# Kernel tuning notes

Hardware: AMD Instinct MI355X
Metric: run time of the kernel (lower is better)

The kernel has to match this reference:

```python
import jax, jax.numpy as jnp
import numpy as np

B, K, R = 16, 256, 256          # batch, text length, encoder dim (r_out_size)
CONV_OUT = 8                    # l_conv_out_size
SW_C = 16                       # l_swish_c_out_size
SW_W = 16                       # l_swish_w_out_size
KS = 3                          # l_conv_kernel_size
T_MAX = 1000                    # torch.clamp(pred_mel_len, max=1000) -> static frame dim
BN_EPS = 1e-5
LN_EPS = 1e-5


def _layer_norm(x, g, b):
    mu = jnp.mean(x, -1, keepdims=True)
    var = jnp.var(x, -1, keepdims=True)
    return (x - mu) * jax.lax.rsqrt(var + LN_EPS) * g + b


def _conv_block(V, w, b, bn_g, bn_b, ln_g, ln_b):
    # ConvBlock: Conv1d(SAME) -> eval BatchNorm (running mean 0 / var 1) -> SiLU -> LayerNorm
    x = jax.lax.conv_general_dilated(V, w, (1,), "SAME",
                                     dimension_numbers=("NWC", "WIO", "NWC")) + b
    x = x * (bn_g / jnp.sqrt(1.0 + BN_EPS)) + bn_b
    x = jax.nn.silu(x)
    return _layer_norm(x, ln_g, ln_b)


def _swish_block(S, E, V8, w1, b1, w2, b2):
    # SwishBlock: Linear(concat([S,E,V8], -1)) -> SiLU -> Linear -> SiLU,
    # without materializing the [B,T,K,CONV_OUT+2] concat (split the first matmul).
    base = V8 @ w1[2:] + b1                                           # [B,K,H]
    h = jax.nn.silu(S[..., None] * w1[0] + E[..., None] * w1[1] + base[:, None])  # [B,T,K,H]
    return jax.nn.silu(h @ w2 + b2)


def setup_inputs():
    key = jax.random.key(0)
    ks = jax.random.split(key, 20)
    f32 = jnp.float32

    inp = {}
    # durations ~ U[0,10): per-utterance sum ~1280 >> T_MAX, so every length clamps to T_MAX
    inp["dur"] = jax.random.uniform(ks[0], (B, K), dtype=f32) * 10.0
    inp["V"] = jax.random.normal(ks[1], (B, K, R), dtype=f32)
    inp["pos_text"] = jnp.tile(jnp.arange(K, dtype=jnp.int32)[None], (B, 1))
    inp["text_mask"] = jnp.zeros((B, K), dtype=bool)

    def n(k, shape, s):
        return jax.random.normal(k, shape, dtype=f32) * s

    for tag, i in (("c", 2), ("w", 6)):
        inp[f"conv_{tag}_w"] = n(ks[i], (KS, R, CONV_OUT), 0.05)
        inp[f"conv_{tag}_b"] = jnp.zeros((CONV_OUT,), f32)
        inp[f"bn_{tag}_g"] = jnp.ones((CONV_OUT,), f32)
        inp[f"bn_{tag}_b"] = jnp.zeros((CONV_OUT,), f32)
        inp[f"ln_{tag}_g"] = jnp.ones((CONV_OUT,), f32)
        inp[f"ln_{tag}_b"] = jnp.zeros((CONV_OUT,), f32)
    inp["swc_w1"] = n(ks[10], (CONV_OUT + 2, SW_C), 0.3)
    inp["swc_b1"] = jnp.zeros((SW_C,), f32)
    inp["swc_w2"] = n(ks[11], (SW_C, SW_C), 0.3)
    inp["swc_b2"] = jnp.zeros((SW_C,), f32)
    inp["sww_w1"] = n(ks[12], (CONV_OUT + 2, SW_W), 0.3)
    inp["sww_b1"] = jnp.zeros((SW_W,), f32)
    inp["sww_w2"] = n(ks[13], (SW_W, SW_W), 0.3)
    inp["sww_b2"] = jnp.zeros((SW_W,), f32)
    inp["proj_w_w"] = n(ks[14], (SW_W, 1), 0.3)
    inp["proj_w_b"] = jnp.zeros((1,), f32)
    inp["lin_e_w"] = n(ks[15], (SW_C, R), 0.1)
    inp["lin_e_b"] = jnp.zeros((R,), f32)
    inp["ln_o_g"] = jnp.ones((R,), f32)
    inp["ln_o_b"] = jnp.zeros((R,), f32)
    return inp


def reference(dur, V, pos_text, text_mask,
              conv_c_w, conv_c_b, bn_c_g, bn_c_b, ln_c_g, ln_c_b,
              conv_w_w, conv_w_b, bn_w_g, bn_w_b, ln_w_g, ln_w_b,
              swc_w1, swc_b1, swc_w2, swc_b2,
              sww_w1, sww_b1, sww_w2, sww_b2,
              proj_w_w, proj_w_b, lin_e_w, lin_e_b, ln_o_g, ln_o_b):
    pred_mel_len = jnp.minimum(jnp.round(dur.sum(-1)), T_MAX).astype(jnp.int32)  # [B]
    pred_mel_mask = jnp.arange(T_MAX, dtype=jnp.int32)[None, :] >= pred_mel_len[:, None]  # [B,T]
    tm = text_mask[:, None, :]       # [B,1,K]
    mm = pred_mel_mask[:, :, None]   # [B,T,1]
    attn_mask = tm | mm              # [B,T,K]

    e_k = jnp.cumsum(dur, axis=1)    # token end boundaries   [B,K]
    s_k = e_k - dur                  # token start boundaries [B,K]
    t = jnp.arange(1, T_MAX + 1, dtype=dur.dtype)[None, :, None]   # frame index [1,T,1]
    S = jnp.where(attn_mask, 0.0, t - s_k[:, None, :])             # [B,T,K]
    E = jnp.where(attn_mask, 0.0, e_k[:, None, :] - t)             # [B,T,K]

    Vw = _conv_block(V, conv_w_w, conv_w_b, bn_w_g, bn_w_b, ln_w_g, ln_w_b)
    Wh = _swish_block(S, E, Vw, sww_w1, sww_b1, sww_w2, sww_b2)    # [B,T,K,SW_W]
    logits = jnp.squeeze(Wh @ proj_w_w, -1) + proj_w_b[0]          # [B,T,K]
    logits = jnp.where(tm, -jnp.inf, logits)
    W = jax.nn.softmax(logits, axis=2)
    W = jnp.where(mm, 0.0, W)

    Vc = _conv_block(V, conv_c_w, conv_c_b, bn_c_g, bn_c_b, ln_c_g, ln_c_b)
    C = _swish_block(S, E, Vc, swc_w1, swc_b1, swc_w2, swc_b2)     # [B,T,K,SW_C]

    agg = jnp.einsum("btk,btkp->btp", W, C)                        # [B,T,SW_C]
    up = jnp.matmul(W, V) + (agg @ lin_e_w + lin_e_b)              # [B,T,R]
    up = _layer_norm(up, ln_o_g, ln_o_b)
    up = jnp.where(pred_mel_mask[..., None], 0.0, up)
    return up, pred_mel_mask, pred_mel_len, W
```

## Files before the change

### kernel.cpp

```cpp
#include <hip/hip_runtime.h>
#include <cstddef>

constexpr int Bn = 16, Kn = 256, Rn = 256, Tn = 1000, C8 = 8, SW = 16;
constexpr size_t UP_SZ    = (size_t)Bn * Tn * Rn;
constexpr size_t MASK_OFF = UP_SZ;
constexpr size_t LEN_OFF  = MASK_OFF + (size_t)Bn * Tn;
constexpr size_t W_OFF    = LEN_OFF + Bn;

using half4_t = __attribute__((ext_vector_type(4))) _Float16;
using f32x4_t = __attribute__((ext_vector_type(4))) float;
using uint2_t = __attribute__((ext_vector_type(2))) unsigned int;

__device__ __forceinline__ float fast_rcp(float x) { return __builtin_amdgcn_rcpf(x); }
__device__ __forceinline__ float fast_exp2(float x) { return __builtin_amdgcn_exp2f(x); }
constexpr float LOG2E = 1.44269504088896340736f;
__device__ __forceinline__ float silu_f(float x) {
    return x * fast_rcp(1.f + fast_exp2(-LOG2E * x));
}

__device__ __forceinline__ void split4(const float x0, const float x1,
                                       const float x2, const float x3,
                                       half4_t& hi, half4_t& lo)
{
    const auto h01 = __builtin_amdgcn_cvt_pkrtz(x0, x1);
    const auto h23 = __builtin_amdgcn_cvt_pkrtz(x2, x3);
    uint2_t uh; uh.x = __builtin_bit_cast(unsigned int, h01);
    uh.y = __builtin_bit_cast(unsigned int, h23);
    hi = __builtin_bit_cast(half4_t, uh);
    const auto l01 = __builtin_amdgcn_cvt_pkrtz(x0 - (float)h01.x, x1 - (float)h01.y);
    const auto l23 = __builtin_amdgcn_cvt_pkrtz(x2 - (float)h23.x, x3 - (float)h23.y);
    uint2_t ul; ul.x = __builtin_bit_cast(unsigned int, l01);
    ul.y = __builtin_bit_cast(unsigned int, l23);
    lo = __builtin_bit_cast(half4_t, ul);
}

__global__ __launch_bounds__(256) void conv_partial_kernel(
    const float* __restrict__ V,
    const float* __restrict__ wW, const float* __restrict__ wC,
    float* __restrict__ part)
{
    const int rc = blockIdx.x, b = blockIdx.y, k = threadIdx.x;
    constexpr int RPAD = 33;
    __shared__ float vt[258 * RPAD];
    if (k < 16) {
        const int row = (k < 8) ? 0 : 257;
        const int j = (k & 7) * 4;
        vt[row * RPAD + j] = 0.f; vt[row * RPAD + j + 1] = 0.f;
        vt[row * RPAD + j + 2] = 0.f; vt[row * RPAD + j + 3] = 0.f;
    }
    const float* vsrc = V + ((size_t)(b * Kn + k)) * Rn + rc * 32;
#pragma unroll
    for (int j = 0; j < 8; j++) {
        const float4 qv = *(const float4*)(vsrc + j * 4);
        float* dst = &vt[(k + 1) * RPAD + j * 4];
        dst[0] = qv.x; dst[1] = qv.y; dst[2] = qv.z; dst[3] = qv.w;
    }
    __syncthreads();

    float aw[C8], ac[C8];
#pragma unroll
    for (int c = 0; c < C8; c++) { aw[c] = 0.f; ac[c] = 0.f; }
    for (int dk = 0; dk < 3; dk++) {
        const float* wp = wW + (size_t)(dk * Rn + rc * 32) * C8;
        const float* cp = wC + (size_t)(dk * Rn + rc * 32) * C8;
        const float* vrow = &vt[(k + dk) * RPAD];
#pragma unroll 4
        for (int r = 0; r < 32; r++) {
            const float v = vrow[r];
#pragma unroll
            for (int c = 0; c < C8; c++) {
                aw[c] = fmaf(v, wp[r * C8 + c], aw[c]);
                ac[c] = fmaf(v, cp[r * C8 + c], ac[c]);
            }
        }
    }
    float* dst = part + ((size_t)(b * 8 + rc) * Kn + k) * 16;
    *(float4*)(dst + 0)  = make_float4(aw[0], aw[1], aw[2], aw[3]);
    *(float4*)(dst + 4)  = make_float4(aw[4], aw[5], aw[6], aw[7]);
    *(float4*)(dst + 8)  = make_float4(ac[0], ac[1], ac[2], ac[3]);
    *(float4*)(dst + 12) = make_float4(ac[4], ac[5], ac[6], ac[7]);
}

__device__ __forceinline__ void conv_post(
    const float* acc, const float* cb, const float* bng, const float* bnb,
    const float* lng, const float* lnb, const float* w1, const float* b1,
    float* __restrict__ dst)
{
    const float bnscale = rsqrtf(1.f + 1e-5f);
    float x[C8];
    float mu = 0.f;
#pragma unroll
    for (int c = 0; c < C8; c++) {
        float v = (acc[c] + cb[c]) * (bng[c] * bnscale) + bnb[c];
        v = silu_f(v);
        x[c] = v; mu += v;
    }
    mu *= (1.f / C8);
    float var = 0.f;
#pragma unroll
    for (int c = 0; c < C8; c++) { float dd = x[c] - mu; var += dd * dd; }
    var *= (1.f / C8);
    const float rs = rsqrtf(var + 1e-5f);
    float y[C8];
#pragma unroll
    for (int c = 0; c < C8; c++) y[c] = (x[c] - mu) * rs * lng[c] + lnb[c];
#pragma unroll
    for (int c2 = 0; c2 < SW; c2++) {
        float a = b1[c2];
#pragma unroll
        for (int p = 0; p < C8; p++) a = fmaf(y[p], w1[(2 + p) * SW + c2], a);
        dst[c2] = a;
    }
}

__global__ __launch_bounds__(256) void conv_scan_finish_kernel(
    const float* __restrict__ dur,
    const float* __restrict__ part,
    const unsigned char* __restrict__ tmask_g,
    const float* __restrict__ bW, const float* __restrict__ bngW, const float* __restrict__ bnbW,
    const float* __restrict__ lngW, const float* __restrict__ lnbW,
    const float* __restrict__ bC, const float* __restrict__ bngC, const float* __restrict__ bnbC,
    const float* __restrict__ lngC, const float* __restrict__ lnbC,
    const float* __restrict__ sww_w1, const float* __restrict__ sww_b1,
    const float* __restrict__ swc_w1, const float* __restrict__ swc_b1,
    float* __restrict__ alpha_ws, float* __restrict__ ab_ws,
    int* __restrict__ len_ws, float* __restrict__ out)
{
    const int b = blockIdx.x, k = threadIdx.x;
    __shared__ float sc[Kn];
    const float d = dur[b * Kn + k];
    sc[k] = d;
    __syncthreads();
    for (int off = 1; off < Kn; off <<= 1) {
        float v = (k >= off) ? sc[k - off] : 0.f;
        __syncthreads();
        sc[k] += v;
        __syncthreads();
    }
    const float ek = sc[k];
    const float sk = ek - d;
    const float total = sc[Kn - 1];
    int len = (int)rintf(total);
    if (len > Tn) len = Tn;
    if (k == 0) { len_ws[b] = len; out[LEN_OFF + b] = (float)len; }
    for (int t = k; t < Tn; t += 256)
        out[MASK_OFF + (size_t)b * Tn + t] = (t >= len) ? 1.f : 0.f;
    if (b == 0 && k < 16) {
        alpha_ws[k]      = sww_w1[k] - sww_w1[SW + k];
        alpha_ws[16 + k] = swc_w1[k] - swc_w1[SW + k];
    }

    float aw[C8], ac[C8];
#pragma unroll
    for (int c = 0; c < C8; c++) { aw[c] = 0.f; ac[c] = 0.f; }
#pragma unroll 2
    for (int rc = 0; rc < 8; rc++) {
        const float4* p = (const float4*)(part + ((size_t)(b * 8 + rc) * Kn + k) * 16);
        const float4 q0 = p[0], q1 = p[1], q2 = p[2], q3 = p[3];
        aw[0] += q0.x; aw[1] += q0.y; aw[2] += q0.z; aw[3] += q0.w;
        aw[4] += q1.x; aw[5] += q1.y; aw[6] += q1.z; aw[7] += q1.w;
        ac[0] += q2.x; ac[1] += q2.y; ac[2] += q2.z; ac[3] += q2.w;
        ac[4] += q3.x; ac[5] += q3.y; ac[6] += q3.z; ac[7] += q3.w;
    }
    float basew[SW], basec[SW];
    conv_post(aw, bW, bngW, bnbW, lngW, lnbW, sww_w1, sww_b1, basew);
    conv_post(ac, bC, bngC, bnbC, lngC, lnbC, swc_w1, swc_b1, basec);

    const bool msk = tmask_g[b * Kn + k] != 0;
    float* dst = ab_ws + ((size_t)(b * Kn) + k) * 32;
#pragma unroll
    for (int c = 0; c < SW; c++) {
        const float w0w = sww_w1[c], w1w_ = sww_w1[SW + c];
        const float w0c = swc_w1[c], w1c_ = swc_w1[SW + c];
        dst[c]      = msk ? basew[c] : fmaf(ek, w1w_, fmaf(-sk, w0w, basew[c]));
        dst[16 + c] = msk ? basec[c] : fmaf(ek, w1c_, fmaf(-sk, w0c, basec[c]));
    }
}

__global__ __launch_bounds__(256) void fused_kernel(
    const unsigned char* __restrict__ tm, const int* __restrict__ len_ws,
    const float* __restrict__ alpha_ws, const float* __restrict__ ab_ws,
    const float* __restrict__ sww_w2, const float* __restrict__ sww_b2,
    const float* __restrict__ proj_w, const float* __restrict__ proj_b,
    const float* __restrict__ swc_w2, const float* __restrict__ swc_b2,
    const float* __restrict__ V,
    const float* __restrict__ lin_e_w, const float* __restrict__ lin_e_b,
    const float* __restrict__ ln_o_g, const float* __restrict__ ln_o_b,
    float* __restrict__ out)
{
    const int t0 = blockIdx.x * 16, b = blockIdx.y, tid = threadIdx.x;
    const int lane = tid & 63, w = tid >> 6, q = lane >> 4, m = lane & 15;
    const int len = len_ws[b];

    __shared__ __align__(16) unsigned int POOL[7680];
    __shared__ __align__(16) float Wl[16 * 256];
    __shared__ __align__(16) float aggp[16][4][16];
    __shared__ float red[8];
    unsigned int* hA = POOL;
    unsigned int* hB = POOL + 2560;
    unsigned int* hC = POOL + 5120;

    float bw[16], bc[16];
    {
        const float4* bp = (const float4*)(ab_ws + (((size_t)b * Kn) + tid) * 32);
#pragma unroll
        for (int i = 0; i < 4; i++) {
            const float4 v = bp[i];
            bw[4*i] = v.x; bw[4*i+1] = v.y; bw[4*i+2] = v.z; bw[4*i+3] = v.w;
        }
#pragma unroll
        for (int i = 0; i < 4; i++) {
            const float4 v = bp[4 + i];
            bc[4*i] = v.x; bc[4*i+1] = v.y; bc[4*i+2] = v.z; bc[4*i+3] = v.w;
        }
    }
    const float mk = (tm[b * Kn + tid] != 0) ? 0.f : 1.f;

    half4_t AWhi, AWlo, ACf;
    float pj[4], b2wv[4], b2cv[4], mb[4];
#pragma unroll
    for (int i = 0; i < 4; i++) {
        const int c = 4 * q + i;
        const float vw = sww_w2[c * SW + m];
        const _Float16 hi = (_Float16)vw;
        AWhi[i] = hi;
        AWlo[i] = (_Float16)(vw - (float)hi);
        ACf[i]  = (_Float16)(swc_w2[c * SW + m]);
        pj[i]   = proj_w[c];
        b2wv[i] = sww_b2[c];
        b2cv[i] = swc_b2[c];
        mb[i]   = (tm[b * Kn + 64 * w + 16 * i + m] != 0) ? -INFINITY : 0.f;
    }
    const float pb = proj_b[0];

    for (int ti = 0; ti < 16; ti++) {
        const int t = t0 + ti;
        if (t >= len) {
            if (t < Tn) out[W_OFF + ((size_t)b * Tn + t) * Kn + tid] = 0.f;
            Wl[ti * 256 + (((tid >> 2) ^ (ti & 7)) << 2) + (tid & 3)] = 0.f;
            continue;
        }
        const float u = (float)(t + 1);
        const float umk = u * mk;

#pragma unroll
        for (int p = 0; p < 8; p++) {
            const float x0 = fmaf(umk, alpha_ws[2*p],   bw[2*p]);
            const float x1 = fmaf(umk, alpha_ws[2*p+1], bw[2*p+1]);
            const float h0 = silu_f(x0), h1 = silu_f(x1);
            const auto hp = __builtin_amdgcn_cvt_pkrtz(h0, h1);
            hA[tid * 10 + p] = __builtin_bit_cast(unsigned int, hp);
            const float l0 = h0 - (float)hp.x, l1 = h1 - (float)hp.y;
            hB[tid * 10 + p] = __builtin_bit_cast(unsigned int,
                                __builtin_amdgcn_cvt_pkrtz(l0, l1));
            const float y0 = fmaf(umk, alpha_ws[16 + 2*p],   bc[2*p]);
            const float y1 = fmaf(umk, alpha_ws[16 + 2*p+1], bc[2*p+1]);
            hC[tid * 10 + p] = __builtin_bit_cast(unsigned int,
                                __builtin_amdgcn_cvt_pkrtz(silu_f(y0), silu_f(y1)));
        }

        f32x4_t o[4];
#pragma unroll
        for (int j = 0; j < 4; j++) {
            const int row = 64 * w + 16 * j + m;
            const uint2_t rh = *(const uint2_t*)&hA[row * 10 + 2 * q];
            const uint2_t rl = *(const uint2_t*)&hB[row * 10 + 2 * q];
            const half4_t bh = __builtin_bit_cast(half4_t, rh);
            const half4_t bl = __builtin_bit_cast(half4_t, rl);
            f32x4_t acc = {0.f, 0.f, 0.f, 0.f};
            acc = __builtin_amdgcn_mfma_f32_16x16x16f16(AWlo, bh, acc, 0, 0, 0);
            acc = __builtin_amdgcn_mfma_f32_16x16x16f16(AWhi, bl, acc, 0, 0, 0);
            acc = __builtin_amdgcn_mfma_f32_16x16x16f16(AWhi, bh, acc, 0, 0, 0);
            o[j] = acc;
        }

        float lg[4];
#pragma unroll
        for (int j = 0; j < 4; j++) {
            float s = silu_f(o[j][0] + b2wv[0]) * pj[0];
            s = fmaf(silu_f(o[j][1] + b2wv[1]), pj[1], s);
            s = fmaf(silu_f(o[j][2] + b2wv[2]), pj[2], s);
            s = fmaf(silu_f(o[j][3] + b2wv[3]), pj[3], s);
            s += __shfl_xor(s, 16, 64);
            s += __shfl_xor(s, 32, 64);
            lg[j] = s + pb + mb[j];
        }

        float mx = fmaxf(fmaxf(lg[0], lg[1]), fmaxf(lg[2], lg[3]));
#pragma unroll
        for (int off = 1; off <= 8; off <<= 1) mx = fmaxf(mx, __shfl_xor(mx, off, 64));
        if (lane == 0) red[w] = mx;
        __syncthreads();
        const float M = fmaxf(fmaxf(red[0], red[1]), fmaxf(red[2], red[3]));
        float pex[4];
#pragma unroll
        for (int j = 0; j < 4; j++) pex[j] = fast_exp2(LOG2E * (lg[j] - M));
        float ssum = (pex[0] + pex[1]) + (pex[2] + pex[3]);
#pragma unroll
        for (int off = 1; off <= 8; off <<= 1) ssum += __shfl_xor(ssum, off, 64);
        if (lane == 0) red[4 + w] = ssum;
        __syncthreads();
        const float inv = fast_rcp(red[4] + red[5] + red[6] + red[7]);
        float wgt[4];
#pragma unroll
        for (int j = 0; j < 4; j++) wgt[j] = pex[j] * inv;
        if (q == 0) {
            float* __restrict__ W_out = out + W_OFF + ((size_t)b * Tn + t) * Kn;
#pragma unroll
            for (int j = 0; j < 4; j++) {
                const int k = 64 * w + 16 * j + m;
                W_out[k] = wgt[j];
                Wl[ti * 256 + ((((k >> 2)) ^ (ti & 7)) << 2) + (k & 3)] = wgt[j];
            }
        }

        f32x4_t ap = {0.f, 0.f, 0.f, 0.f};
#pragma unroll
        for (int j = 0; j < 4; j++) {
            const int row = 64 * w + 16 * j + m;
            const uint2_t rc2 = *(const uint2_t*)&hC[row * 10 + 2 * q];
            f32x4_t zz = {0.f, 0.f, 0.f, 0.f};
            const f32x4_t oc = __builtin_amdgcn_mfma_f32_16x16x16f16(
                ACf, __builtin_bit_cast(half4_t, rc2), zz, 0, 0, 0);
#pragma unroll
            for (int i = 0; i < 4; i++)
                ap[i] = fmaf(silu_f(oc[i] + b2cv[i]), wgt[j], ap[i]);
        }
#pragma unroll
        for (int off = 1; off <= 8; off <<= 1) {
            ap[0] += __shfl_xor(ap[0], off, 64);
            ap[1] += __shfl_xor(ap[1], off, 64);
            ap[2] += __shfl_xor(ap[2], off, 64);
            ap[3] += __shfl_xor(ap[3], off, 64);
        }
        if (m == 0)
            *(float4*)&aggp[ti][w][4 * q] = make_float4(ap[0], ap[1], ap[2], ap[3]);
    }
    __syncthreads();

    f32x4_t acc[4];
#pragma unroll
    for (int i = 0; i < 4; i++) acc[i] = f32x4_t{0.f, 0.f, 0.f, 0.f};
    const float* Vb = V + (size_t)b * Kn * Rn;

#pragma unroll
    for (int ks = 0; ks < 16; ks++) {
        const float4 wv = *(const float4*)&Wl[m * 256 + (((4 * ks + q) ^ (m & 7)) << 2)];
        half4_t Ahi, Alo;
        split4(wv.x, wv.y, wv.z, wv.w, Ahi, Alo);
        const float* vp = Vb + (size_t)(ks * 16 + 4 * q) * Rn;
#pragma unroll
        for (int rt = 0; rt < 4; rt++) {
            const int rcol = w * 64 + rt * 16 + m;
            const float b0 = vp[rcol],          b1 = vp[Rn + rcol];
            const float b2 = vp[2 * Rn + rcol], b3 = vp[3 * Rn + rcol];
            half4_t Bh, Bl;
            split4(b0, b1, b2, b3, Bh, Bl);
            acc[rt] = __builtin_amdgcn_mfma_f32_16x16x16f16(Alo, Bh, acc[rt], 0, 0, 0);
            acc[rt] = __builtin_amdgcn_mfma_f32_16x16x16f16(Ahi, Bl, acc[rt], 0, 0, 0);
            acc[rt] = __builtin_amdgcn_mfma_f32_16x16x16f16(Ahi, Bh, acc[rt], 0, 0, 0);
        }
    }
    float* raw = (float*)POOL;
#pragma unroll
    for (int rt = 0; rt < 4; rt++) {
#pragma unroll
        for (int i = 0; i < 4; i++)
            raw[(4 * q + i) * 260 + w * 64 + rt * 16 + m] = acc[rt][i];
    }
    __syncthreads();

#pragma unroll
    for (int j = 0; j < 4; j++) {
        const int tl = 4 * w + j;
        const int t = t0 + tl;
        if (t >= Tn) continue;
        float* __restrict__ row = out + ((size_t)b * Tn + t) * Rn;
        const int r0 = lane * 4;
        if (t >= len) {
            *(float4*)(row + r0) = make_float4(0.f, 0.f, 0.f, 0.f);
            continue;
        }
        float4 a4 = *(const float4*)&raw[tl * 260 + r0];
        {
            const float4 be = *(const float4*)(lin_e_b + r0);
            a4.x += be.x; a4.y += be.y; a4.z += be.z; a4.w += be.w;
        }
#pragma unroll
        for (int p = 0; p < 16; p++) {
            const float a = aggp[tl][0][p] + aggp[tl][1][p] + aggp[tl][2][p] + aggp[tl][3][p];
            const float4 l = *(const float4*)(lin_e_w + p * Rn + r0);
            a4.x = fmaf(a, l.x, a4.x); a4.y = fmaf(a, l.y, a4.y);
            a4.z = fmaf(a, l.z, a4.z); a4.w = fmaf(a, l.w, a4.w);
        }
        float s = (a4.x + a4.y) + (a4.z + a4.w);
#pragma unroll
        for (int off = 1; off <= 32; off <<= 1) s += __shfl_xor(s, off, 64);
        const float mu = s * (1.f / Rn);
        const float d0 = a4.x - mu, d1 = a4.y - mu, d2 = a4.z - mu, d3 = a4.w - mu;
        float vr = d0 * d0 + d1 * d1 + d2 * d2 + d3 * d3;
#pragma unroll
        for (int off = 1; off <= 32; off <<= 1) vr += __shfl_xor(vr, off, 64);
        const float rs = rsqrtf(vr * (1.f / Rn) + 1e-5f);
        const float4 g = *(const float4*)(ln_o_g + r0);
        const float4 bb = *(const float4*)(ln_o_b + r0);
        float4 res;
        res.x = d0 * rs * g.x + bb.x;
        res.y = d1 * rs * g.y + bb.y;
        res.z = d2 * rs * g.z + bb.z;
        res.w = d3 * rs * g.w + bb.w;
        *(float4*)(row + r0) = res;
    }
}

extern "C" void kernel_launch(void* const* d_in, const int* in_sizes, int n_in,
                              void* d_out, int out_size, void* d_ws, size_t ws_size,
                              hipStream_t stream)
{
    const float* dur       = (const float*)d_in[0];
    const float* V         = (const float*)d_in[1];
    const unsigned char* text_mask = (const unsigned char*)d_in[3];
    const float* conv_c_w  = (const float*)d_in[4];
    const float* conv_c_b  = (const float*)d_in[5];
    const float* bn_c_g    = (const float*)d_in[6];
    const float* bn_c_b    = (const float*)d_in[7];
    const float* ln_c_g    = (const float*)d_in[8];
    const float* ln_c_b    = (const float*)d_in[9];
    const float* conv_w_w  = (const float*)d_in[10];
    const float* conv_w_b  = (const float*)d_in[11];
    const float* bn_w_g    = (const float*)d_in[12];
    const float* bn_w_b    = (const float*)d_in[13];
    const float* ln_w_g    = (const float*)d_in[14];
    const float* ln_w_b    = (const float*)d_in[15];
    const float* swc_w1    = (const float*)d_in[16];
    const float* swc_b1    = (const float*)d_in[17];
    const float* swc_w2    = (const float*)d_in[18];
    const float* swc_b2    = (const float*)d_in[19];
    const float* sww_w1    = (const float*)d_in[20];
    const float* sww_b1    = (const float*)d_in[21];
    const float* sww_w2    = (const float*)d_in[22];
    const float* sww_b2    = (const float*)d_in[23];
    const float* proj_w_w  = (const float*)d_in[24];
    const float* proj_w_b  = (const float*)d_in[25];
    const float* lin_e_w   = (const float*)d_in[26];
    const float* lin_e_b   = (const float*)d_in[27];
    const float* ln_o_g    = (const float*)d_in[28];
    const float* ln_o_b    = (const float*)d_in[29];

    float* out = (float*)d_out;
    float* wsf = (float*)d_ws;
    int*   len_ws   = (int*)wsf;
    float* alpha_ws = wsf + 64;
    float* ab_ws    = wsf + 128;
    float* part     = ab_ws + 131072;

    conv_partial_kernel<<<dim3(8, Bn), dim3(256), 0, stream>>>(V, conv_w_w, conv_c_w, part);
    conv_scan_finish_kernel<<<dim3(Bn), dim3(256), 0, stream>>>(
        dur, part, text_mask,
        conv_w_b, bn_w_g, bn_w_b, ln_w_g, ln_w_b,
        conv_c_b, bn_c_g, bn_c_b, ln_c_g, ln_c_b,
        sww_w1, sww_b1, swc_w1, swc_b1,
        alpha_ws, ab_ws, len_ws, out);
    fused_kernel<<<dim3((Tn + 15) / 16, Bn), dim3(256), 0, stream>>>(
        text_mask, len_ws, alpha_ws, ab_ws,
        sww_w2, sww_b2, proj_w_w, proj_w_b,
        swc_w2, swc_b2,
        V, lin_e_w, lin_e_b, ln_o_g, ln_o_b, out);
}
```

Measured before the change: 164.8 us.

## Split fused kernel into logits/softmax kernel and W·V matvec+layernorm kernel

Splits the single fused kernel in two. The first computes the swish MLPs, the softmax weights and the aggregated context per frame over 8-frame tiles, which doubles the block count. It double-buffers the aggregation partials so each frame needs one fewer barrier, and writes agg to workspace. The second kernel reloads W from global output, does the W·V MFMA matvec, adds the lin_e projection and applies layernorm. This aims at better occupancy and a smaller LDS footprint per kernel, at the cost of an extra launch and a round trip of W and agg through global memory.

```diff
diff --git a/kernel.cpp b/kernel.cpp
--- a/kernel.cpp
+++ b/kernel.cpp
@@ -177,28 +177,23 @@
     }
 }
 
-__global__ __launch_bounds__(256) void fused_kernel(
+__global__ __launch_bounds__(256) void logits_kernel(
     const unsigned char* __restrict__ tm, const int* __restrict__ len_ws,
     const float* __restrict__ alpha_ws, const float* __restrict__ ab_ws,
     const float* __restrict__ sww_w2, const float* __restrict__ sww_b2,
     const float* __restrict__ proj_w, const float* __restrict__ proj_b,
     const float* __restrict__ swc_w2, const float* __restrict__ swc_b2,
-    const float* __restrict__ V,
-    const float* __restrict__ lin_e_w, const float* __restrict__ lin_e_b,
-    const float* __restrict__ ln_o_g, const float* __restrict__ ln_o_b,
-    float* __restrict__ out)
-{
-    const int t0 = blockIdx.x * 16, b = blockIdx.y, tid = threadIdx.x;
+    float* __restrict__ agg_ws, float* __restrict__ out)
+{
+    const int t0 = blockIdx.x * 8, b = blockIdx.y, tid = threadIdx.x;
     const int lane = tid & 63, w = tid >> 6, q = lane >> 4, m = lane & 15;
     const int len = len_ws[b];
 
-    __shared__ __align__(16) unsigned int POOL[7680];
-    __shared__ __align__(16) float Wl[16 * 256];
-    __shared__ __align__(16) float aggp[16][4][16];
+    __shared__ __align__(16) unsigned int hA[256 * 10];
+    __shared__ __align__(16) unsigned int hB[256 * 10];
+    __shared__ __align__(16) unsigned int hC[256 * 10];
     __shared__ float red[8];
-    unsigned int* hA = POOL;
-    unsigned int* hB = POOL + 2560;
-    unsigned int* hC = POOL + 5120;
+    __shared__ __align__(16) float aggw[2][4][16];
 
     float bw[16], bc[16];
     {
@@ -233,13 +228,12 @@
     }
     const float pb = proj_b[0];
 
-    for (int ti = 0; ti < 16; ti++) {
+    int pend = -1, pendpar = 0;
+
+    for (int ti = 0; ti < 8; ti++) {
         const int t = t0 + ti;
-        if (t >= len) {
-            if (t < Tn) out[W_OFF + ((size_t)b * Tn + t) * Kn + tid] = 0.f;
-            Wl[ti * 256 + (((tid >> 2) ^ (ti & 7)) << 2) + (tid & 3)] = 0.f;
-            continue;
-        }
+        float* __restrict__ W_out = out + W_OFF + ((size_t)b * Tn + t) * Kn;
+        if (t >= len) { W_out[tid] = 0.f; continue; }
         const float u = (float)(t + 1);
         const float umk = u * mk;
 
@@ -291,6 +285,13 @@
         for (int off = 1; off <= 8; off <<= 1) mx = fmaxf(mx, __shfl_xor(mx, off, 64));
         if (lane == 0) red[w] = mx;
         __syncthreads();
+        if (pend >= 0) {
+            if (tid < 16)
+                agg_ws[((size_t)b * Tn + pend) * 16 + tid] =
+                    aggw[pendpar][0][tid] + aggw[pendpar][1][tid] +
+                    aggw[pendpar][2][tid] + aggw[pendpar][3][tid];
+            pend = -1;
+        }
         const float M = fmaxf(fmaxf(red[0], red[1]), fmaxf(red[2], red[3]));
         float pex[4];
 #pragma unroll
@@ -305,13 +306,8 @@
 #pragma unroll
         for (int j = 0; j < 4; j++) wgt[j] = pex[j] * inv;
         if (q == 0) {
-            float* __restrict__ W_out = out + W_OFF + ((size_t)b * Tn + t) * Kn;
-#pragma unroll
-            for (int j = 0; j < 4; j++) {
-                const int k = 64 * w + 16 * j + m;
-                W_out[k] = wgt[j];
-                Wl[ti * 256 + ((((k >> 2)) ^ (ti & 7)) << 2) + (k & 3)] = wgt[j];
-            }
+#pragma unroll
+            for (int j = 0; j < 4; j++) W_out[64 * w + 16 * j + m] = wgt[j];
         }
 
         f32x4_t ap = {0.f, 0.f, 0.f, 0.f};
@@ -334,7 +330,41 @@
             ap[3] += __shfl_xor(ap[3], off, 64);
         }
         if (m == 0)
-            *(float4*)&aggp[ti][w][4 * q] = make_float4(ap[0], ap[1], ap[2], ap[3]);
+            *(float4*)&aggw[ti & 1][w][4 * q] = make_float4(ap[0], ap[1], ap[2], ap[3]);
+        pend = t; pendpar = ti & 1;
+    }
+    if (pend >= 0) {
+        __syncthreads();
+        if (tid < 16)
+            agg_ws[((size_t)b * Tn + pend) * 16 + tid] =
+                aggw[pendpar][0][tid] + aggw[pendpar][1][tid] +
+                aggw[pendpar][2][tid] + aggw[pendpar][3][tid];
+    }
+}
+
+__global__ __launch_bounds__(256) void matvec_ln_kernel(
+    const float* __restrict__ Wg, const float* __restrict__ V,
+    const float* __restrict__ agg_ws, const int* __restrict__ len_ws,
+    const float* __restrict__ lin_e_w, const float* __restrict__ lin_e_b,
+    const float* __restrict__ ln_o_g, const float* __restrict__ ln_o_b,
+    float* __restrict__ out)
+{
+    const int t0 = blockIdx.x * 16, b = blockIdx.y, tid = threadIdx.x;
+    const int lane = tid & 63, w = tid >> 6, q = lane >> 4, m = lane & 15;
+    const int len = len_ws[b];
+
+    __shared__ __align__(16) float Wl[16 * 256];
+    __shared__ __align__(16) float raw[16 * 260];
+
+    const float4* Wg4 = (const float4*)Wg;
+#pragma unroll
+    for (int ch = 0; ch < 4; ch++) {
+        const int idx = ch * 256 + tid;
+        const int row = idx >> 6, sl = idx & 63;
+        const int t = t0 + row;
+        const float4 v = (t < Tn) ? Wg4[((size_t)b * Tn + t) * 64 + sl]
+                                  : make_float4(0.f, 0.f, 0.f, 0.f);
+        *(float4*)&Wl[row * 256 + ((sl ^ (row & 7)) << 2)] = v;
     }
     __syncthreads();
 
@@ -361,7 +391,6 @@
             acc[rt] = __builtin_amdgcn_mfma_f32_16x16x16f16(Ahi, Bh, acc[rt], 0, 0, 0);
         }
     }
-    float* raw = (float*)POOL;
 #pragma unroll
     for (int rt = 0; rt < 4; rt++) {
 #pragma unroll
@@ -386,9 +415,10 @@
             const float4 be = *(const float4*)(lin_e_b + r0);
             a4.x += be.x; a4.y += be.y; a4.z += be.z; a4.w += be.w;
         }
+        const float* aggp = agg_ws + ((size_t)b * Tn + t) * 16;
 #pragma unroll
         for (int p = 0; p < 16; p++) {
-            const float a = aggp[tl][0][p] + aggp[tl][1][p] + aggp[tl][2][p] + aggp[tl][3][p];
+            const float a = aggp[p];
             const float4 l = *(const float4*)(lin_e_w + p * Rn + r0);
             a4.x = fmaf(a, l.x, a4.x); a4.y = fmaf(a, l.y, a4.y);
             a4.z = fmaf(a, l.z, a4.z); a4.w = fmaf(a, l.w, a4.w);
@@ -452,7 +482,9 @@
     int*   len_ws   = (int*)wsf;
     float* alpha_ws = wsf + 64;
     float* ab_ws    = wsf + 128;
-    float* part     = ab_ws + 131072;
+    float* scratch  = ab_ws + 131072;
+    float* part     = scratch;
+    float* agg_ws   = scratch;
 
     conv_partial_kernel<<<dim3(8, Bn), dim3(256), 0, stream>>>(V, conv_w_w, conv_c_w, part);
     conv_scan_finish_kernel<<<dim3(Bn), dim3(256), 0, stream>>>(
@@ -461,9 +493,12 @@
         conv_c_b, bn_c_g, bn_c_b, ln_c_g, ln_c_b,
         sww_w1, sww_b1, swc_w1, swc_b1,
         alpha_ws, ab_ws, len_ws, out);
-    fused_kernel<<<dim3((Tn + 15) / 16, Bn), dim3(256), 0, stream>>>(
+    logits_kernel<<<dim3(Tn / 8, Bn), dim3(256), 0, stream>>>(
         text_mask, len_ws, alpha_ws, ab_ws,
         sww_w2, sww_b2, proj_w_w, proj_w_b,
         swc_w2, swc_b2,
-        V, lin_e_w, lin_e_b, ln_o_g, ln_o_b, out);
-}
+        agg_ws, out);
+    matvec_ln_kernel<<<dim3((Tn + 15) / 16, Bn), dim3(256), 0, stream>>>(
+        out + W_OFF, V, agg_ws, len_ws,
+        lin_e_w, lin_e_b, ln_o_g, ln_o_b, out);
+}
```

Measured after the change: 160.3 us. -2.7%, faster.
